# Kernel optimization log

Measured on AMD Instinct MI355X. Metric: run time of the kernel, lower is better.

## Reference

```python
import jax, jax.numpy as jnp
import numpy as np

ENC2 = 1024   # encoder_hidden_dim * 2
DEC = 1024    # decoder_hidden_dim
ATT = 512     # attention_dim
B, S = 32, 2048


def setup_inputs() -> dict:
    key = jax.random.key(0)
    ks = jax.random.split(key, 7)
    sW = 1.0 / np.sqrt(DEC)
    sU = 1.0 / np.sqrt(ENC2)
    sv = 1.0 / np.sqrt(ATT)
    return {
        "decoder_hidden": jax.random.normal(ks[0], (B, DEC), jnp.float32),
        "encoder_all_hidden": jax.random.normal(ks[1], (B, S, ENC2), jnp.float32),
        "W_w": jax.random.uniform(ks[2], (DEC, ATT), jnp.float32, -sW, sW),
        "W_b": jax.random.uniform(ks[3], (ATT,), jnp.float32, -sW, sW),
        "U_w": jax.random.uniform(ks[4], (ENC2, ATT), jnp.float32, -sU, sU),
        "U_b": jax.random.uniform(ks[5], (ATT,), jnp.float32, -sU, sU),
        "v_w": jax.random.uniform(ks[6], (ATT, 1), jnp.float32, -sv, sv),
    }


def reference(decoder_hidden, encoder_all_hidden, W_w, W_b, U_w, U_b, v_w):
    # Ws: (B, 1, A); Uh: (B, S, A)
    Ws = (decoder_hidden @ W_w + W_b)[:, None, :]
    Uh = jnp.einsum('bse,ea->bsa', encoder_all_hidden, U_w) + U_b
    energy = jnp.einsum('bsa,ao->bs', jnp.tanh(Ws + Uh), v_w)
    alpha = jax.nn.softmax(energy, axis=1)
    return alpha
```

## Files before the change

### kernel.cpp

```cpp
#include <hip/hip_runtime.h>
#include <hip/hip_bf16.h>
#include <math.h>

#define ENC2 1024
#define DECD 1024
#define ATT 512
#define NBATCH 32
#define SEQ 2048
#define MTOT (NBATCH*SEQ)

#define BM 128
#define BN2 256
#define BK 32
#define LDK 40

typedef __attribute__((ext_vector_type(8))) short short8;
typedef __attribute__((ext_vector_type(4))) short short4v;
typedef __attribute__((ext_vector_type(4))) float f32x4;

static __device__ __forceinline__ unsigned pk2(float a, float b) {
  __hip_bfloat162 h = __float22bfloat162_rn(float2{a, b});
  union { __hip_bfloat162 h; unsigned u; } c; c.h = h;
  return c.u;
}

static __device__ __forceinline__ float fast_tanh(float x) {
  float ax = fabsf(x);
  float e = __expf(2.f * ax);
  float t = 1.f - 2.f / (e + 1.f);
  return copysignf(t, x);
}

__global__ __launch_bounds__(256) void uwT_kernel(const float* __restrict__ U_w,
                                                  short* __restrict__ U_wT) {
  __shared__ float tile[64][65];
  const int kt = blockIdx.x >> 3;
  const int ct = blockIdx.x & 7;
  const int k0 = kt * 64, c0 = ct * 64;
  const int t = threadIdx.x;
  const int r = t >> 4, cc = (t & 15) * 4;
  #pragma unroll
  for (int p = 0; p < 4; p++) {
    float4 v = *(const float4*)(U_w + (size_t)(k0 + r + p*16) * ATT + c0 + cc);
    tile[r + p*16][cc+0] = v.x; tile[r + p*16][cc+1] = v.y;
    tile[r + p*16][cc+2] = v.z; tile[r + p*16][cc+3] = v.w;
  }
  __syncthreads();
  const int cr = t >> 4, kk = (t & 15) * 4;
  #pragma unroll
  for (int p = 0; p < 4; p++) {
    int c = cr + p*16;
    unsigned u0 = pk2(tile[kk + 0][c], tile[kk + 1][c]);
    unsigned u1 = pk2(tile[kk + 2][c], tile[kk + 3][c]);
    union { short4v s; unsigned u[2]; } o; o.u[0] = u0; o.u[1] = u1;
    *(short4v*)(U_wT + (size_t)(c0 + c) * ENC2 + k0 + kk) = o.s;
  }
}

__global__ __launch_bounds__(512) void ws_kernel(const float* __restrict__ dh,
                                                 const float* __restrict__ W_w,
                                                 const float* __restrict__ W_b,
                                                 const float* __restrict__ U_b,
                                                 float* __restrict__ Wsb) {
  __shared__ float dsh[DECD];
  __shared__ float part[4][ATT];
  const int b = blockIdx.x;
  const int t = threadIdx.x;
  for (int i = t; i < DECD; i += 512) dsh[i] = dh[(size_t)b * DECD + i];
  __syncthreads();
  const int ks = t >> 7;
  const int a4 = (t & 127) * 4;
  const float* wp = W_w + (size_t)(ks * 256) * ATT + a4;
  float4 s = {0.f, 0.f, 0.f, 0.f};
  #pragma unroll 8
  for (int k = 0; k < 256; k++) {
    float4 wv = *(const float4*)(wp + (size_t)k * ATT);
    float d = dsh[ks * 256 + k];
    s.x = fmaf(d, wv.x, s.x); s.y = fmaf(d, wv.y, s.y);
    s.z = fmaf(d, wv.z, s.z); s.w = fmaf(d, wv.w, s.w);
  }
  *(float4*)&part[ks][a4] = s;
  __syncthreads();
  if (t < ATT) {
    float v = part[0][t] + part[1][t] + part[2][t] + part[3][t];
    Wsb[(size_t)b * ATT + t] = v + W_b[t] + U_b[t];
  }
}

__global__ __launch_bounds__(512) void energy_kernel(
    const float* __restrict__ A,
    const short* __restrict__ Bt,
    const float* __restrict__ Wsb,
    const float* __restrict__ vw,
    float* __restrict__ epart)
{
  __shared__ __align__(16) short As[2][BM * LDK];
  __shared__ __align__(16) short Bs[2][BN2 * LDK];
  __shared__ float eps[4][BM];

  const int tid = threadIdx.x;
  const int bid = blockIdx.x;
  const int mt = (bid >> 4) * 8 + (bid & 7);
  const int nt = (bid >> 3) & 1;
  const int row0 = mt * BM;
  const int col0 = nt * BN2;
  const int bidx = row0 / SEQ;

  const int lane = tid & 63;
  const int wid  = tid >> 6;
  const int wm   = wid >> 2;
  const int wn   = wid & 3;

  const int ar = tid >> 2, ak = (tid & 3) * 8;
  const int bc = tid >> 1, bk = (tid & 1) * 16;

  const int fr = lane & 15;
  const int k0 = (lane >> 4) * 8;

  f32x4 acc[4][4];
  #pragma unroll
  for (int m = 0; m < 4; m++)
    #pragma unroll
    for (int n = 0; n < 4; n++) acc[m][n] = (f32x4){0.f, 0.f, 0.f, 0.f};

  const float* Abase = A + (size_t)row0 * ENC2;
  const short* Bbase = Bt + (size_t)col0 * ENC2;

  float4 aR0, aR1;
  short8 bR0, bR1;

  aR0 = *(const float4*)(Abase + (size_t)ar * ENC2 + ak);
  aR1 = *(const float4*)(Abase + (size_t)ar * ENC2 + ak + 4);
  bR0 = *(const short8*)(Bbase + (size_t)bc * ENC2 + bk);
  bR1 = *(const short8*)(Bbase + (size_t)bc * ENC2 + bk + 8);
  {
    union { short8 s; unsigned u[4]; } w;
    w.u[0] = pk2(aR0.x, aR0.y); w.u[1] = pk2(aR0.z, aR0.w);
    w.u[2] = pk2(aR1.x, aR1.y); w.u[3] = pk2(aR1.z, aR1.w);
    *(short8*)(&As[0][ar * LDK + ak]) = w.s;
    *(short8*)(&Bs[0][bc * LDK + bk]) = bR0;
    *(short8*)(&Bs[0][bc * LDK + bk + 8]) = bR1;
  }
  __syncthreads();

  const int NT = ENC2 / BK;
  for (int kt = 0; kt < NT; kt++) {
    const int cur = kt & 1;
    const bool more = (kt + 1 < NT);
    if (more) {
      const float* Ab = Abase + (kt + 1) * BK;
      aR0 = *(const float4*)(Ab + (size_t)ar * ENC2 + ak);
      aR1 = *(const float4*)(Ab + (size_t)ar * ENC2 + ak + 4);
      const short* Bb = Bbase + (kt + 1) * BK;
      bR0 = *(const short8*)(Bb + (size_t)bc * ENC2 + bk);
      bR1 = *(const short8*)(Bb + (size_t)bc * ENC2 + bk + 8);
    }
    short8 af[4], bfr[4];
    #pragma unroll
    for (int m = 0; m < 4; m++)
      af[m] = *(const short8*)(&As[cur][(wm*64 + m*16 + fr) * LDK + k0]);
    #pragma unroll
    for (int n = 0; n < 4; n++)
      bfr[n] = *(const short8*)(&Bs[cur][(wn*64 + n*16 + fr) * LDK + k0]);
    #pragma unroll
    for (int m = 0; m < 4; m++)
      #pragma unroll
      for (int n = 0; n < 4; n++)
        acc[m][n] = __builtin_amdgcn_mfma_f32_16x16x32_bf16(af[m], bfr[n], acc[m][n], 0, 0, 0);
    if (more) {
      union { short8 s; unsigned u[4]; } w;
      w.u[0] = pk2(aR0.x, aR0.y); w.u[1] = pk2(aR0.z, aR0.w);
      w.u[2] = pk2(aR1.x, aR1.y); w.u[3] = pk2(aR1.z, aR1.w);
      *(short8*)(&As[cur ^ 1][ar * LDK + ak]) = w.s;
      *(short8*)(&Bs[cur ^ 1][bc * LDK + bk]) = bR0;
      *(short8*)(&Bs[cur ^ 1][bc * LDK + bk + 8]) = bR1;
    }
    __syncthreads();
  }

  float vv[4], wsb[4];
  #pragma unroll
  for (int n = 0; n < 4; n++) {
    const int gc = col0 + wn*64 + n*16 + fr;
    vv[n]  = vw[gc];
    wsb[n] = Wsb[(size_t)bidx * ATT + gc];
  }
  const int rg = lane >> 4;
  #pragma unroll
  for (int m = 0; m < 4; m++) {
    float part[4] = {0.f, 0.f, 0.f, 0.f};
    #pragma unroll
    for (int n = 0; n < 4; n++) {
      #pragma unroll
      for (int r = 0; r < 4; r++)
        part[r] += vv[n] * fast_tanh(acc[m][n][r] + wsb[n]);
    }
    #pragma unroll
    for (int r = 0; r < 4; r++) {
      float p = part[r];
      p += __shfl_xor(p, 1);
      p += __shfl_xor(p, 2);
      p += __shfl_xor(p, 4);
      p += __shfl_xor(p, 8);
      if (fr == 0) eps[wn][wm*64 + m*16 + rg*4 + r] = p;
    }
  }
  __syncthreads();
  if (tid < BM) {
    float s = eps[0][tid] + eps[1][tid] + eps[2][tid] + eps[3][tid];
    epart[(size_t)nt * MTOT + row0 + tid] = s;
  }
}

__global__ __launch_bounds__(256) void softmax_kernel(const float* __restrict__ epart,
                                                      float* __restrict__ out) {
  __shared__ float redmax[4];
  __shared__ float redsum[4];
  const int b = blockIdx.x, t = threadIdx.x;
  const float* e0 = epart + (size_t)b * SEQ;
  const float* e1 = epart + (size_t)MTOT + (size_t)b * SEQ;
  float vals[8];
  float mx = -1e30f;
  #pragma unroll
  for (int i = 0; i < 8; i++) {
    vals[i] = e0[t + i*256] + e1[t + i*256];
    mx = fmaxf(mx, vals[i]);
  }
  #pragma unroll
  for (int off = 1; off < 64; off <<= 1) mx = fmaxf(mx, __shfl_xor(mx, off));
  if ((t & 63) == 0) redmax[t >> 6] = mx;
  __syncthreads();
  mx = fmaxf(fmaxf(redmax[0], redmax[1]), fmaxf(redmax[2], redmax[3]));
  float sum = 0.f;
  #pragma unroll
  for (int i = 0; i < 8; i++) { vals[i] = expf(vals[i] - mx); sum += vals[i]; }
  #pragma unroll
  for (int off = 1; off < 64; off <<= 1) sum += __shfl_xor(sum, off);
  if ((t & 63) == 0) redsum[t >> 6] = sum;
  __syncthreads();
  const float inv = 1.f / (redsum[0] + redsum[1] + redsum[2] + redsum[3]);
  #pragma unroll
  for (int i = 0; i < 8; i++) out[(size_t)b * SEQ + t + i*256] = vals[i] * inv;
}

extern "C" void kernel_launch(void* const* d_in, const int* in_sizes, int n_in,
                              void* d_out, int out_size, void* d_ws, size_t ws_size,
                              hipStream_t stream) {
  const float* dh  = (const float*)d_in[0];
  const float* enc = (const float*)d_in[1];
  const float* W_w = (const float*)d_in[2];
  const float* W_b = (const float*)d_in[3];
  const float* U_w = (const float*)d_in[4];
  const float* U_b = (const float*)d_in[5];
  const float* v_w = (const float*)d_in[6];
  float* out = (float*)d_out;

  char* ws = (char*)d_ws;
  float* epart = (float*)ws;
  float* Wsb   = (float*)(ws + 512 * 1024);
  short* U_wT  = (short*)(ws + 576 * 1024);

  uwT_kernel<<<128, 256, 0, stream>>>(U_w, U_wT);
  ws_kernel<<<NBATCH, 512, 0, stream>>>(dh, W_w, W_b, U_b, Wsb);
  energy_kernel<<<1024, 512, 0, stream>>>(enc, U_wT, Wsb, v_w, epart);
  softmax_kernel<<<NBATCH, 256, 0, stream>>>(epart, out);
}
```

Measured before the change: 154.4 us.

## Load B fragments directly into registers, drop B LDS staging, widen ws grid

The energy GEMM no longer stages the bf16 U_w^T tile in shared memory. Each wave now loads its own B MFMA fragments straight from global memory into double-buffered registers, and only the A tile goes through LDS. This cuts LDS use and shared-memory traffic, and adds a min-blocks hint of 4 to raise occupancy, at the cost of redundant global B loads across the two wave rows and higher register pressure. The ws_kernel is also split four ways across the attention dimension so that 128 blocks run instead of 32.

```diff
diff --git a/kernel.cpp b/kernel.cpp
--- a/kernel.cpp
+++ b/kernel.cpp
@@ -63,39 +63,69 @@
                                                  const float* __restrict__ U_b,
                                                  float* __restrict__ Wsb) {
   __shared__ float dsh[DECD];
-  __shared__ float part[4][ATT];
-  const int b = blockIdx.x;
+  __shared__ float part[4][128];
+  const int b  = blockIdx.x >> 2;
+  const int a0 = (blockIdx.x & 3) * 128;
   const int t = threadIdx.x;
   for (int i = t; i < DECD; i += 512) dsh[i] = dh[(size_t)b * DECD + i];
   __syncthreads();
   const int ks = t >> 7;
-  const int a4 = (t & 127) * 4;
-  const float* wp = W_w + (size_t)(ks * 256) * ATT + a4;
-  float4 s = {0.f, 0.f, 0.f, 0.f};
-  #pragma unroll 8
-  for (int k = 0; k < 256; k++) {
-    float4 wv = *(const float4*)(wp + (size_t)k * ATT);
-    float d = dsh[ks * 256 + k];
-    s.x = fmaf(d, wv.x, s.x); s.y = fmaf(d, wv.y, s.y);
-    s.z = fmaf(d, wv.z, s.z); s.w = fmaf(d, wv.w, s.w);
-  }
-  *(float4*)&part[ks][a4] = s;
-  __syncthreads();
-  if (t < ATT) {
+  const int a  = t & 127;
+  const float* wp = W_w + (size_t)(ks * 256) * ATT + a0 + a;
+  float s0 = 0.f, s1 = 0.f, s2 = 0.f, s3 = 0.f;
+  #pragma unroll 4
+  for (int kk = 0; kk < 256; kk += 4) {
+    s0 = fmaf(dsh[ks*256 + kk + 0], wp[(size_t)(kk + 0) * ATT], s0);
+    s1 = fmaf(dsh[ks*256 + kk + 1], wp[(size_t)(kk + 1) * ATT], s1);
+    s2 = fmaf(dsh[ks*256 + kk + 2], wp[(size_t)(kk + 2) * ATT], s2);
+    s3 = fmaf(dsh[ks*256 + kk + 3], wp[(size_t)(kk + 3) * ATT], s3);
+  }
+  part[ks][a] = (s0 + s1) + (s2 + s3);
+  __syncthreads();
+  if (t < 128) {
     float v = part[0][t] + part[1][t] + part[2][t] + part[3][t];
-    Wsb[(size_t)b * ATT + t] = v + W_b[t] + U_b[t];
-  }
-}
-
-__global__ __launch_bounds__(512) void energy_kernel(
+    Wsb[(size_t)b * ATT + a0 + t] = v + W_b[a0 + t] + U_b[a0 + t];
+  }
+}
+
+#define K_STEP(KT, RBUF, WBUF, BUSE, BLOAD, MORE)                              \
+  do {                                                                         \
+    float4 aR0, aR1;                                                           \
+    if (MORE) {                                                                \
+      const float* Ab = Aptr + (KT + 1) * BK;                                  \
+      aR0 = *(const float4*)(Ab);                                              \
+      aR1 = *(const float4*)(Ab + 4);                                          \
+      BLOAD[0] = *(const short8*)(bp0 + (KT + 1) * BK);                        \
+      BLOAD[1] = *(const short8*)(bp1 + (KT + 1) * BK);                        \
+      BLOAD[2] = *(const short8*)(bp2 + (KT + 1) * BK);                        \
+      BLOAD[3] = *(const short8*)(bp3 + (KT + 1) * BK);                        \
+    }                                                                          \
+    _Pragma("unroll")                                                          \
+    for (int m = 0; m < 4; m++) {                                              \
+      short8 af = *(const short8*)(&RBUF[(wm*64 + m*16 + fr) * LDK + k0]);     \
+      acc[m][0] = __builtin_amdgcn_mfma_f32_16x16x32_bf16(af, BUSE[0], acc[m][0], 0, 0, 0); \
+      acc[m][1] = __builtin_amdgcn_mfma_f32_16x16x32_bf16(af, BUSE[1], acc[m][1], 0, 0, 0); \
+      acc[m][2] = __builtin_amdgcn_mfma_f32_16x16x32_bf16(af, BUSE[2], acc[m][2], 0, 0, 0); \
+      acc[m][3] = __builtin_amdgcn_mfma_f32_16x16x32_bf16(af, BUSE[3], acc[m][3], 0, 0, 0); \
+    }                                                                          \
+    if (MORE) {                                                                \
+      union { short8 s; unsigned u[4]; } w;                                    \
+      w.u[0] = pk2(aR0.x, aR0.y); w.u[1] = pk2(aR0.z, aR0.w);                  \
+      w.u[2] = pk2(aR1.x, aR1.y); w.u[3] = pk2(aR1.z, aR1.w);                  \
+      *(short8*)(&WBUF[ar * LDK + ak]) = w.s;                                  \
+    }                                                                          \
+    __syncthreads();                                                           \
+  } while (0)
+
+__global__ __launch_bounds__(512, 4) void energy_kernel(
     const float* __restrict__ A,
     const short* __restrict__ Bt,
     const float* __restrict__ Wsb,
     const float* __restrict__ vw,
     float* __restrict__ epart)
 {
-  __shared__ __align__(16) short As[2][BM * LDK];
-  __shared__ __align__(16) short Bs[2][BN2 * LDK];
+  __shared__ __align__(16) short As0[BM * LDK];
+  __shared__ __align__(16) short As1[BM * LDK];
   __shared__ float eps[4][BM];
 
   const int tid = threadIdx.x;
@@ -112,7 +142,6 @@
   const int wn   = wid & 3;
 
   const int ar = tid >> 2, ak = (tid & 3) * 8;
-  const int bc = tid >> 1, bk = (tid & 1) * 16;
 
   const int fr = lane & 15;
   const int k0 = (lane >> 4) * 8;
@@ -123,59 +152,31 @@
     #pragma unroll
     for (int n = 0; n < 4; n++) acc[m][n] = (f32x4){0.f, 0.f, 0.f, 0.f};
 
-  const float* Abase = A + (size_t)row0 * ENC2;
-  const short* Bbase = Bt + (size_t)col0 * ENC2;
-
-  float4 aR0, aR1;
-  short8 bR0, bR1;
-
-  aR0 = *(const float4*)(Abase + (size_t)ar * ENC2 + ak);
-  aR1 = *(const float4*)(Abase + (size_t)ar * ENC2 + ak + 4);
-  bR0 = *(const short8*)(Bbase + (size_t)bc * ENC2 + bk);
-  bR1 = *(const short8*)(Bbase + (size_t)bc * ENC2 + bk + 8);
+  const float* Aptr = A + (size_t)row0 * ENC2 + (size_t)ar * ENC2 + ak;
+  const short* bp0 = Bt + (size_t)(col0 + wn*64 +  0 + fr) * ENC2 + k0;
+  const short* bp1 = Bt + (size_t)(col0 + wn*64 + 16 + fr) * ENC2 + k0;
+  const short* bp2 = Bt + (size_t)(col0 + wn*64 + 32 + fr) * ENC2 + k0;
+  const short* bp3 = Bt + (size_t)(col0 + wn*64 + 48 + fr) * ENC2 + k0;
+
+  short8 b0[4], b1[4];
+
+  b0[0] = *(const short8*)(bp0);
+  b0[1] = *(const short8*)(bp1);
+  b0[2] = *(const short8*)(bp2);
+  b0[3] = *(const short8*)(bp3);
   {
+    float4 aR0 = *(const float4*)(Aptr);
+    float4 aR1 = *(const float4*)(Aptr + 4);
     union { short8 s; unsigned u[4]; } w;
     w.u[0] = pk2(aR0.x, aR0.y); w.u[1] = pk2(aR0.z, aR0.w);
     w.u[2] = pk2(aR1.x, aR1.y); w.u[3] = pk2(aR1.z, aR1.w);
-    *(short8*)(&As[0][ar * LDK + ak]) = w.s;
-    *(short8*)(&Bs[0][bc * LDK + bk]) = bR0;
-    *(short8*)(&Bs[0][bc * LDK + bk + 8]) = bR1;
-  }
-  __syncthreads();
-
-  const int NT = ENC2 / BK;
-  for (int kt = 0; kt < NT; kt++) {
-    const int cur = kt & 1;
-    const bool more = (kt + 1 < NT);
-    if (more) {
-      const float* Ab = Abase + (kt + 1) * BK;
-      aR0 = *(const float4*)(Ab + (size_t)ar * ENC2 + ak);
-      aR1 = *(const float4*)(Ab + (size_t)ar * ENC2 + ak + 4);
-      const short* Bb = Bbase + (kt + 1) * BK;
-      bR0 = *(const short8*)(Bb + (size_t)bc * ENC2 + bk);
-      bR1 = *(const short8*)(Bb + (size_t)bc * ENC2 + bk + 8);
-    }
-    short8 af[4], bfr[4];
-    #pragma unroll
-    for (int m = 0; m < 4; m++)
-      af[m] = *(const short8*)(&As[cur][(wm*64 + m*16 + fr) * LDK + k0]);
-    #pragma unroll
-    for (int n = 0; n < 4; n++)
-      bfr[n] = *(const short8*)(&Bs[cur][(wn*64 + n*16 + fr) * LDK + k0]);
-    #pragma unroll
-    for (int m = 0; m < 4; m++)
-      #pragma unroll
-      for (int n = 0; n < 4; n++)
-        acc[m][n] = __builtin_amdgcn_mfma_f32_16x16x32_bf16(af[m], bfr[n], acc[m][n], 0, 0, 0);
-    if (more) {
-      union { short8 s; unsigned u[4]; } w;
-      w.u[0] = pk2(aR0.x, aR0.y); w.u[1] = pk2(aR0.z, aR0.w);
-      w.u[2] = pk2(aR1.x, aR1.y); w.u[3] = pk2(aR1.z, aR1.w);
-      *(short8*)(&As[cur ^ 1][ar * LDK + ak]) = w.s;
-      *(short8*)(&Bs[cur ^ 1][bc * LDK + bk]) = bR0;
-      *(short8*)(&Bs[cur ^ 1][bc * LDK + bk + 8]) = bR1;
-    }
-    __syncthreads();
+    *(short8*)(&As0[ar * LDK + ak]) = w.s;
+  }
+  __syncthreads();
+
+  for (int k2 = 0; k2 < 32; k2 += 2) {
+    K_STEP(k2,     As0, As1, b0, b1, true);
+    K_STEP(k2 + 1, As1, As0, b1, b0, (k2 + 1) < 31);
   }
 
   float vv[4], wsb[4];
@@ -261,7 +262,7 @@
   short* U_wT  = (short*)(ws + 576 * 1024);
 
   uwT_kernel<<<128, 256, 0, stream>>>(U_w, U_wT);
-  ws_kernel<<<NBATCH, 512, 0, stream>>>(dh, W_w, W_b, U_b, Wsb);
+  ws_kernel<<<128, 512, 0, stream>>>(dh, W_w, W_b, U_b, Wsb);
   energy_kernel<<<1024, 512, 0, stream>>>(enc, U_wT, Wsb, v_w, epart);
   softmax_kernel<<<NBATCH, 256, 0, stream>>>(epart, out);
 }
```

Result: slower. 184.9 us (+19.7%).
